# Performance work log

Measured on AMD Instinct MI355X. Metric: run time of the kernel, lower is better.

Reference implementation:

```python
import jax, jax.numpy as jnp
import numpy as np

HIDDEN = 1024
INTER = 2048
NUM_EXPERTS = 8
TOP_K = 2
GROUP_SIZE = 128
TOKENS = 4096


def _dequant_int4(packed, scale, group_size):
    # packed: [E, N, K//2] ints in [0,256) holding two uint4 nibbles (low | high<<4)
    # scale:  [E, N, K//group_size] float32
    E, N, Kh = packed.shape
    K = 2 * Kh
    low = packed & 0xF
    high = (packed >> 4) & 0xF
    # interleave: even K positions = low nibble, odd = high nibble
    q = jnp.stack([low, high], axis=-1).reshape(E, N, K) - 8  # int4 values in [-8,7]
    q = q.astype(jnp.float32).reshape(E, N, K // group_size, group_size)
    w = q * scale[..., None]
    return w.reshape(E, N, K)


def setup_inputs() -> dict:
    key = jax.random.key(0)
    k1, k2, k3, k4, k5, k6 = jax.random.split(key, 6)
    x = jax.random.normal(k1, (TOKENS, HIDDEN), dtype=jnp.float32)
    router_w = jax.random.normal(k2, (NUM_EXPERTS, HIDDEN), dtype=jnp.float32) * 0.02
    w1 = jax.random.randint(k3, (NUM_EXPERTS, 2 * INTER, HIDDEN // 2), 0, 256, dtype=jnp.int32)
    w1_scale = jax.random.uniform(k4, (NUM_EXPERTS, 2 * INTER, HIDDEN // GROUP_SIZE), dtype=jnp.float32) * 0.05
    w2 = jax.random.randint(k5, (NUM_EXPERTS, HIDDEN, INTER // 2), 0, 256, dtype=jnp.int32)
    w2_scale = jax.random.uniform(k6, (NUM_EXPERTS, HIDDEN, INTER // GROUP_SIZE), dtype=jnp.float32) * 0.05
    return {"x": x, "router_w": router_w, "w1": w1, "w1_scale": w1_scale, "w2": w2, "w2_scale": w2_scale}


def reference(x, router_w, w1, w1_scale, w2, w2_scale):
    # Router: topk then softmax over the top-k logits
    scores = x @ router_w.T                                 # [T, E]
    top_w, top_i = jax.lax.top_k(scores, TOP_K)             # [T, K]
    top_w = jax.nn.softmax(top_w, axis=-1).astype(jnp.float32)

    # Dequantize int4 grouped weights once
    w1_deq = _dequant_int4(w1, w1_scale, GROUP_SIZE)        # [E, 2I, H]
    w2_deq = _dequant_int4(w2, w2_scale, GROUP_SIZE)        # [E, H, I]

    out = jnp.zeros_like(x)
    for e in range(NUM_EXPERTS):
        # per-token routing weight for expert e (0 if not routed)
        ge = jnp.sum(top_w * (top_i == e), axis=-1)         # [T]
        h = x @ w1_deq[e].T                                  # [T, 2I]
        gate, up = h[:, :INTER], h[:, INTER:]
        a = jax.nn.silu(gate) * up                           # SwiGLU
        y = a @ w2_deq[e].T                                  # [T, H]
        out = out + ge[:, None] * y
    return out
```

## Files before the change

### kernel.cpp

```cpp
#include <hip/hip_runtime.h>
#include <hip/hip_bf16.h>

#define HIDDEN 1024
#define INTER 2048
#define NE 8
#define GS 128
#define TOKENS 4096
#define MAXROWS 9216
#define MAXTILES 72

typedef __bf16 bf16x8 __attribute__((ext_vector_type(8)));
typedef float f32x4 __attribute__((ext_vector_type(4)));

#define OFF_TOPKI 0u
#define OFF_TOPKW 32768u
#define OFF_CTRL  65536u
#define OFF_TOK   66048u
#define OFF_SLOT  102912u
#define OFF_TILE  135680u
#define OFF_XB    139776u
#define OFF_A     8530432u
#define OFF_W1D   46279168u
#define OFF_W2D   113388032u
#define OFF_Y0    OFF_W1D
#define OFF_Y1    (OFF_W1D + 18874368u)

__device__ __forceinline__ unsigned short f2bf(float f) {
  union { float f; unsigned int u; } v; v.f = f;
  unsigned int r = (v.u + 0x7FFFu + ((v.u >> 16) & 1u)) >> 16;
  return (unsigned short)r;
}
__device__ __forceinline__ float bf2f(unsigned int u) {
  union { unsigned int u; float f; } v; v.u = u << 16;
  return v.f;
}
__device__ __forceinline__ unsigned int pack2(unsigned short lo, unsigned short hi) {
  return (unsigned int)lo | ((unsigned int)hi << 16);
}

typedef const __attribute__((address_space(1))) unsigned int GAS;
typedef __attribute__((address_space(3))) unsigned int LAS;
__device__ __forceinline__ void gload16(const unsigned short* g, unsigned short* l) {
  __builtin_amdgcn_global_load_lds((GAS*)g, (LAS*)l, 16, 0, 0);
}


__global__ __launch_bounds__(256) void k_prep(const float* __restrict__ x,
    const float* __restrict__ rw, int* __restrict__ topki, float* __restrict__ topkw,
    const int* __restrict__ w1, const float* __restrict__ w1s,
    unsigned short* __restrict__ w1d,
    const int* __restrict__ w2, const float* __restrict__ w2s,
    unsigned short* __restrict__ w2d, unsigned short* __restrict__ xb) {
  int bid = blockIdx.x, tid = threadIdx.x;
  if (bid == 29696) {
    uint2 z; z.x = 0u; z.y = 0u;
    *reinterpret_cast<uint2*>(xb + (size_t)TOKENS * HIDDEN + tid * 4) = z;
    return;
  }
  if (bid >= 25600) {
    size_t idx = (size_t)(bid - 25600) * 1024 + tid * 4;
    float4 v = *reinterpret_cast<const float4*>(x + idx);
    uint2 o;
    o.x = pack2(f2bf(v.x), f2bf(v.y));
    o.y = pack2(f2bf(v.z), f2bf(v.w));
    *reinterpret_cast<uint2*>(xb + idx) = o;
    return;
  }
  if (bid >= 17408) {
    int gid = (bid - 17408) * 256 + tid;
    int i4 = gid * 4;
    int r = i4 >> 10;
    int i = i4 & 1023;
    float s = w2s[r * 16 + (i >> 6)];
    int4 p = *reinterpret_cast<const int4*>(w2 + (size_t)i4);
    int pv[4] = { p.x, p.y, p.z, p.w };
    uint4 o; unsigned int ov[4];
#pragma unroll
    for (int j = 0; j < 4; j++) {
      float lo = (float)((pv[j] & 15) - 8) * s;
      float hi = (float)(((pv[j] >> 4) & 15) - 8) * s;
      ov[j] = pack2(f2bf(lo), f2bf(hi));
    }
    o.x = ov[0]; o.y = ov[1]; o.z = ov[2]; o.w = ov[3];
    *reinterpret_cast<uint4*>(w2d + ((size_t)r << 11) + 2 * i) = o;
    return;
  }
  if (bid >= 1024) {
    int gid = (bid - 1024) * 256 + tid;
    int i4 = gid * 4;
    int r = i4 >> 9;
    int i = i4 & 511;
    float s = w1s[r * 8 + (i >> 6)];
    int4 p = *reinterpret_cast<const int4*>(w1 + (size_t)i4);
    int pv[4] = { p.x, p.y, p.z, p.w };
    uint4 o; unsigned int ov[4];
#pragma unroll
    for (int j = 0; j < 4; j++) {
      float lo = (float)((pv[j] & 15) - 8) * s;
      float hi = (float)(((pv[j] >> 4) & 15) - 8) * s;
      ov[j] = pack2(f2bf(lo), f2bf(hi));
    }
    o.x = ov[0]; o.y = ov[1]; o.z = ov[2]; o.w = ov[3];
    *reinterpret_cast<uint4*>(w1d + ((size_t)r << 10) + 2 * i) = o;
    return;
  }
  int wave = tid >> 6, lane = tid & 63;
  int t = bid * 4 + wave;
  float acc[NE];
#pragma unroll
  for (int e = 0; e < NE; e++) acc[e] = 0.f;
  const float* xr = x + (size_t)t * HIDDEN;
  for (int i = lane; i < HIDDEN; i += 64) {
    float xv = xr[i];
#pragma unroll
    for (int e = 0; e < NE; e++) acc[e] += xv * rw[e * HIDDEN + i];
  }
#pragma unroll
  for (int e = 0; e < NE; e++) {
    float v = acc[e];
    for (int off = 32; off > 0; off >>= 1) v += __shfl_down(v, off, 64);
    acc[e] = v;
  }
  if (lane == 0) {
    int b0 = 0; float s0 = acc[0];
#pragma unroll
    for (int e = 1; e < NE; e++) if (acc[e] > s0) { s0 = acc[e]; b0 = e; }
    int b1 = -1; float s1 = -3.0e38f;
#pragma unroll
    for (int e = 0; e < NE; e++) if (e != b0 && acc[e] > s1) { s1 = acc[e]; b1 = e; }
    float w0 = 1.f / (1.f + __expf(s1 - s0));
    topki[t * 2] = b0; topki[t * 2 + 1] = b1;
    topkw[t * 2] = w0; topkw[t * 2 + 1] = 1.f - w0;
  }
}

__global__ __launch_bounds__(256) void k_route2(const int* __restrict__ topki,
    int* __restrict__ ctrl, int* __restrict__ tok, int* __restrict__ slots,
    int* __restrict__ tilemap) {
  __shared__ int h[NE], off[NE], cnt[NE];
  int tid = threadIdx.x;
  if (tid < NE) h[tid] = 0;
  __syncthreads();
  for (int i = tid; i < TOKENS * 2; i += 256) atomicAdd(&h[topki[i]], 1);
  __syncthreads();
  if (tid == 0) {
    int run = 0, t = 0;
    for (int e = 0; e < NE; e++) {
      int c = h[e];
      ctrl[e] = c; ctrl[16 + e] = run; off[e] = run;
      int pc = (c + 127) & ~127;
      for (int mt = 0; mt < (pc >> 7); mt++) tilemap[t++] = (e << 20) | (run + mt * 128);
      run += pc;
    }
    ctrl[24] = run; ctrl[25] = t;
  }
  __syncthreads();
#pragma unroll
  for (int e = 0; e < NE; e++) {
    int c = h[e], pc = (c + 127) & ~127;
    for (int i = c + tid; i < pc; i += 256) tok[off[e] + i] = -1;
  }
  if (tid < NE) cnt[tid] = off[tid];
  __syncthreads();
  for (int i = tid; i < TOKENS * 2; i += 256) {
    int e = topki[i];
    int p = atomicAdd(&cnt[e], 1);
    tok[p] = i >> 1;
    slots[i] = p;
  }
}

__global__ __launch_bounds__(256) void k_gemm1(
    const unsigned short* __restrict__ xb, const unsigned short* __restrict__ w1d,
    const int* __restrict__ ctrl, const int* __restrict__ tilemap,
    const int* __restrict__ tok, unsigned short* __restrict__ a_out) {
  __shared__ unsigned short sA[128 * 32];
  __shared__ unsigned short sBg[64 * 32];
  __shared__ unsigned short sBu[64 * 32];
  int bid = blockIdx.x, tid = threadIdx.x;
  int nt = bid & 31, tile = bid >> 5;
  if (tile >= ctrl[25]) return;
  int tm = tilemap[tile];
  int e = tm >> 20, row0 = tm & 0xFFFFF;
  int n0 = nt * 64;
  int wave = tid >> 6, lane = tid & 63;
  int ln = lane & 15, quad = lane >> 4;
  int wr = (wave & 1) * 64, wc = (wave >> 1) * 32;

  int srow = tid >> 2, scblk = tid & 3;
  int scol = (scblk ^ ((srow >> 1) & 3)) * 8;
  int t0 = tok[row0 + srow];
  int t1 = tok[row0 + 64 + srow];
  const unsigned short* gA0 = xb + (size_t)(t0 < 0 ? TOKENS : t0) * HIDDEN + scol;
  const unsigned short* gA1 = xb + (size_t)(t1 < 0 ? TOKENS : t1) * HIDDEN + scol;
  const unsigned short* gBg = w1d + ((size_t)e * 4096 + n0 + srow) * HIDDEN + scol;
  const unsigned short* gBu = gBg + (size_t)INTER * HIDDEN;
  unsigned short* lA0 = sA + tid * 8;
  unsigned short* lA1 = sA + 64 * 32 + tid * 8;
  unsigned short* lBg = sBg + tid * 8;
  unsigned short* lBu = sBu + tid * 8;

  f32x4 aG[4][2] = {}, aU[4][2] = {};
  for (int k0 = 0; k0 < HIDDEN; k0 += 32) {
    __syncthreads();
    gload16(gA0 + k0, lA0);
    gload16(gA1 + k0, lA1);
    gload16(gBg + k0, lBg);
    gload16(gBu + k0, lBu);
    __syncthreads();
    bf16x8 af[4], bg[2], bu[2];
#pragma unroll
    for (int m = 0; m < 4; m++) {
      int ar = wr + m * 16 + ln;
      af[m] = *reinterpret_cast<const bf16x8*>(&sA[ar * 32 + (quad ^ ((ar >> 1) & 3)) * 8]);
    }
#pragma unroll
    for (int n = 0; n < 2; n++) {
      int br = wc + n * 16 + ln;
      int bo = br * 32 + (quad ^ ((br >> 1) & 3)) * 8;
      bg[n] = *reinterpret_cast<const bf16x8*>(&sBg[bo]);
      bu[n] = *reinterpret_cast<const bf16x8*>(&sBu[bo]);
    }
#pragma unroll
    for (int m = 0; m < 4; m++)
#pragma unroll
      for (int n = 0; n < 2; n++) {
        aG[m][n] = __builtin_amdgcn_mfma_f32_16x16x32_bf16(af[m], bg[n], aG[m][n], 0, 0, 0);
        aU[m][n] = __builtin_amdgcn_mfma_f32_16x16x32_bf16(af[m], bu[n], aU[m][n], 0, 0, 0);
      }
  }
#pragma unroll
  for (int m = 0; m < 4; m++)
#pragma unroll
    for (int n = 0; n < 2; n++) {
      int col = n0 + wc + n * 16 + ln;
#pragma unroll
      for (int r = 0; r < 4; r++) {
        float g = aG[m][n][r], u = aU[m][n][r];
        float act = (g / (1.f + __expf(-g))) * u;
        int row = row0 + wr + m * 16 + quad * 4 + r;
        a_out[(size_t)row * INTER + col] = f2bf(act);
      }
    }
}

__global__ __launch_bounds__(256) void k_gemm2(
    const unsigned short* __restrict__ a_in, const unsigned short* __restrict__ w2d,
    const int* __restrict__ ctrl, const int* __restrict__ tilemap,
    unsigned short* __restrict__ y) {
  __shared__ unsigned short sA[128 * 32];
  __shared__ unsigned short sB[128 * 32];
  int bid = blockIdx.x, tid = threadIdx.x;
  int kp = bid & 1, nt = (bid >> 1) & 7, tile = bid >> 4;
  if (tile >= ctrl[25]) return;
  int tm = tilemap[tile];
  int e = tm >> 20, row0 = tm & 0xFFFFF;
  int n0 = nt * 128;
  int wave = tid >> 6, lane = tid & 63;
  int ln = lane & 15, quad = lane >> 4;
  int wr = (wave & 1) * 64, wc = (wave >> 1) * 64;

  int srow = tid >> 2, scblk = tid & 3;
  int scol = (scblk ^ ((srow >> 1) & 3)) * 8;
  int kbase = kp * (INTER / 2);
  const unsigned short* gA0 = a_in + (size_t)(row0 + srow) * INTER + kbase + scol;
  const unsigned short* gA1 = gA0 + (size_t)64 * INTER;
  const unsigned short* gB0 = w2d + ((size_t)e * 1024 + n0 + srow) * INTER + kbase + scol;
  const unsigned short* gB1 = gB0 + (size_t)64 * INTER;
  unsigned short* lA0 = sA + tid * 8;
  unsigned short* lA1 = sA + 64 * 32 + tid * 8;
  unsigned short* lB0 = sB + tid * 8;
  unsigned short* lB1 = sB + 64 * 32 + tid * 8;

  f32x4 acc[4][4] = {};
  for (int k0 = 0; k0 < INTER / 2; k0 += 32) {
    __syncthreads();
    gload16(gA0 + k0, lA0);
    gload16(gA1 + k0, lA1);
    gload16(gB0 + k0, lB0);
    gload16(gB1 + k0, lB1);
    __syncthreads();
    bf16x8 af[4], bf_[4];
#pragma unroll
    for (int m = 0; m < 4; m++) {
      int ar = wr + m * 16 + ln;
      af[m] = *reinterpret_cast<const bf16x8*>(&sA[ar * 32 + (quad ^ ((ar >> 1) & 3)) * 8]);
    }
#pragma unroll
    for (int n = 0; n < 4; n++) {
      int br = wc + n * 16 + ln;
      bf_[n] = *reinterpret_cast<const bf16x8*>(&sB[br * 32 + (quad ^ ((br >> 1) & 3)) * 8]);
    }
#pragma unroll
    for (int m = 0; m < 4; m++)
#pragma unroll
      for (int n = 0; n < 4; n++)
        acc[m][n] = __builtin_amdgcn_mfma_f32_16x16x32_bf16(af[m], bf_[n], acc[m][n], 0, 0, 0);
  }
  unsigned short* yk = y + (size_t)kp * MAXROWS * HIDDEN;
#pragma unroll
  for (int m = 0; m < 4; m++)
#pragma unroll
    for (int n = 0; n < 4; n++) {
      int col = n0 + wc + n * 16 + ln;
#pragma unroll
      for (int r = 0; r < 4; r++) {
        int row = row0 + wr + m * 16 + quad * 4 + r;
        yk[(size_t)row * HIDDEN + col] = f2bf(acc[m][n][r]);
      }
    }
}

__global__ __launch_bounds__(256) void k_combine(const unsigned short* __restrict__ y,
    const int* __restrict__ slots, const float* __restrict__ topkw,
    float* __restrict__ out) {
  int t = blockIdx.x;
  int c = threadIdx.x * 4;
  int s0 = slots[t * 2], s1 = slots[t * 2 + 1];
  float g0 = topkw[t * 2], g1 = topkw[t * 2 + 1];
  const unsigned short* y1 = y + (size_t)MAXROWS * HIDDEN;
  uint2 a0 = *reinterpret_cast<const uint2*>(y  + (size_t)s0 * HIDDEN + c);
  uint2 a1 = *reinterpret_cast<const uint2*>(y1 + (size_t)s0 * HIDDEN + c);
  uint2 b0 = *reinterpret_cast<const uint2*>(y  + (size_t)s1 * HIDDEN + c);
  uint2 b1 = *reinterpret_cast<const uint2*>(y1 + (size_t)s1 * HIDDEN + c);
  float4 o;
  o.x = g0 * (bf2f(a0.x & 0xffffu) + bf2f(a1.x & 0xffffu))
      + g1 * (bf2f(b0.x & 0xffffu) + bf2f(b1.x & 0xffffu));
  o.y = g0 * (bf2f(a0.x >> 16) + bf2f(a1.x >> 16))
      + g1 * (bf2f(b0.x >> 16) + bf2f(b1.x >> 16));
  o.z = g0 * (bf2f(a0.y & 0xffffu) + bf2f(a1.y & 0xffffu))
      + g1 * (bf2f(b0.y & 0xffffu) + bf2f(b1.y & 0xffffu));
  o.w = g0 * (bf2f(a0.y >> 16) + bf2f(a1.y >> 16))
      + g1 * (bf2f(b0.y >> 16) + bf2f(b1.y >> 16));
  *reinterpret_cast<float4*>(out + (size_t)t * HIDDEN + c) = o;
}

extern "C" void kernel_launch(void* const* d_in, const int* in_sizes, int n_in,
                              void* d_out, int out_size, void* d_ws, size_t ws_size,
                              hipStream_t stream) {
  const float* x   = (const float*)d_in[0];
  const float* rw  = (const float*)d_in[1];
  const int*   w1  = (const int*)d_in[2];
  const float* w1s = (const float*)d_in[3];
  const int*   w2  = (const int*)d_in[4];
  const float* w2s = (const float*)d_in[5];
  float* out = (float*)d_out;
  char* ws = (char*)d_ws;

  int*   topki = (int*)(ws + OFF_TOPKI);
  float* topkw = (float*)(ws + OFF_TOPKW);
  int*   ctrl  = (int*)(ws + OFF_CTRL);
  int*   tok   = (int*)(ws + OFF_TOK);
  int*   slots = (int*)(ws + OFF_SLOT);
  int*   tilemap = (int*)(ws + OFF_TILE);
  unsigned short* xb  = (unsigned short*)(ws + OFF_XB);
  unsigned short* a   = (unsigned short*)(ws + OFF_A);
  unsigned short* w1d = (unsigned short*)(ws + OFF_W1D);
  unsigned short* w2d = (unsigned short*)(ws + OFF_W2D);
  unsigned short* y   = (unsigned short*)(ws + OFF_Y0);

  k_prep<<<29697, 256, 0, stream>>>(x, rw, topki, topkw, w1, w1s, w1d, w2, w2s, w2d, xb);
  k_route2<<<1, 256, 0, stream>>>(topki, ctrl, tok, slots, tilemap);
  k_gemm1<<<32 * MAXTILES, 256, 0, stream>>>(xb, w1d, ctrl, tilemap, tok, a);
  k_gemm2<<<16 * MAXTILES, 256, 0, stream>>>(a, w2d, ctrl, tilemap, y);
  k_combine<<<TOKENS, 256, 0, stream>>>(y, slots, topkw, out);
}
```

Before: 324.5 us.

## Rewrite gemm1 as 256x256 pipelined tile with interleaved gate/up weights

Replaces the 128x64 gemm1 tile with a 512-thread 256x256 tile. It double-buffers LDS, issues prefetches two k-steps ahead and uses setprio around the MFMA phases. The w1 dequant now interleaves gate and up rows in blocks of 16, so one B tile covers both halves, and 256-row tiles per expert are handled with a valid-row count. Routing histogram counting moves into k_prep via global atomics, and token scatter moves to a new multi-block kernel. Together these aim for more reuse per tile, latency hiding and less serial routing work, at the cost of padding waste on partial tiles and more complex synchronization.

```diff
diff --git a/kernel.cpp b/kernel.cpp
--- a/kernel.cpp
+++ b/kernel.cpp
@@ -8,6 +8,7 @@
 #define TOKENS 4096
 #define MAXROWS 9216
 #define MAXTILES 72
+#define MAXT256 40
 
 typedef __bf16 bf16x8 __attribute__((ext_vector_type(8)));
 typedef float f32x4 __attribute__((ext_vector_type(4)));
@@ -18,6 +19,8 @@
 #define OFF_TOK   66048u
 #define OFF_SLOT  102912u
 #define OFF_TILE  135680u
+#define OFF_T256  136192u
+#define OFF_V256  136448u
 #define OFF_XB    139776u
 #define OFF_A     8530432u
 #define OFF_W1D   46279168u
@@ -44,13 +47,13 @@
   __builtin_amdgcn_global_load_lds((GAS*)g, (LAS*)l, 16, 0, 0);
 }
 
-
 __global__ __launch_bounds__(256) void k_prep(const float* __restrict__ x,
     const float* __restrict__ rw, int* __restrict__ topki, float* __restrict__ topkw,
     const int* __restrict__ w1, const float* __restrict__ w1s,
     unsigned short* __restrict__ w1d,
     const int* __restrict__ w2, const float* __restrict__ w2s,
-    unsigned short* __restrict__ w2d, unsigned short* __restrict__ xb) {
+    unsigned short* __restrict__ w2d, unsigned short* __restrict__ xb,
+    int* __restrict__ ctrl) {
   int bid = blockIdx.x, tid = threadIdx.x;
   if (bid == 29696) {
     uint2 z; z.x = 0u; z.y = 0u;
@@ -101,7 +104,11 @@
       ov[j] = pack2(f2bf(lo), f2bf(hi));
     }
     o.x = ov[0]; o.y = ov[1]; o.z = ov[2]; o.w = ov[3];
-    *reinterpret_cast<uint4*>(w1d + ((size_t)r << 10) + 2 * i) = o;
+    int e = r >> 12, rr = r & 4095;
+    int tp = rr >> 11, jj = rr & 2047;
+    int il = ((jj >> 4) << 5) + (tp << 4) + (jj & 15);
+    size_t orow = ((size_t)e << 12) + il;
+    *reinterpret_cast<uint4*>(w1d + (orow << 10) + 2 * i) = o;
     return;
   }
   int wave = tid >> 6, lane = tid & 63;
@@ -131,28 +138,38 @@
     float w0 = 1.f / (1.f + __expf(s1 - s0));
     topki[t * 2] = b0; topki[t * 2 + 1] = b1;
     topkw[t * 2] = w0; topkw[t * 2 + 1] = 1.f - w0;
-  }
-}
-
-__global__ __launch_bounds__(256) void k_route2(const int* __restrict__ topki,
-    int* __restrict__ ctrl, int* __restrict__ tok, int* __restrict__ slots,
-    int* __restrict__ tilemap) {
-  __shared__ int h[NE], off[NE], cnt[NE];
+    atomicAdd(&ctrl[b0], 1);
+    atomicAdd(&ctrl[b1], 1);
+  }
+}
+
+__global__ __launch_bounds__(256) void k_route2(int* __restrict__ ctrl,
+    int* __restrict__ tok, int* __restrict__ tilemap,
+    int* __restrict__ tile256, int* __restrict__ valid256) {
+  __shared__ int h[NE], off[NE];
   int tid = threadIdx.x;
-  if (tid < NE) h[tid] = 0;
-  __syncthreads();
-  for (int i = tid; i < TOKENS * 2; i += 256) atomicAdd(&h[topki[i]], 1);
+  if (tid < NE) h[tid] = ctrl[tid];
   __syncthreads();
   if (tid == 0) {
-    int run = 0, t = 0;
+    int run = 0, t = 0, t2 = 0;
     for (int e = 0; e < NE; e++) {
       int c = h[e];
-      ctrl[e] = c; ctrl[16 + e] = run; off[e] = run;
+      ctrl[16 + e] = run; off[e] = run;
+      ctrl[8 + e] = run;
       int pc = (c + 127) & ~127;
-      for (int mt = 0; mt < (pc >> 7); mt++) tilemap[t++] = (e << 20) | (run + mt * 128);
+      int m = pc >> 7;
+      for (int mt = 0; mt < m; mt++) tilemap[t++] = (e << 20) | (run + mt * 128);
+      int n2 = (m + 1) >> 1;
+      for (int i = 0; i < n2; i++) {
+        int st = i * 256;
+        if (st + 256 > pc) st = (pc >= 256) ? (pc - 256) : 0;
+        tile256[t2] = (e << 20) | (run + st);
+        int v = pc - st; valid256[t2] = (v < 256) ? v : 256;
+        t2++;
+      }
       run += pc;
     }
-    ctrl[24] = run; ctrl[25] = t;
+    ctrl[24] = run; ctrl[25] = t; ctrl[26] = t2;
   }
   __syncthreads();
 #pragma unroll
@@ -160,88 +177,168 @@
     int c = h[e], pc = (c + 127) & ~127;
     for (int i = c + tid; i < pc; i += 256) tok[off[e] + i] = -1;
   }
-  if (tid < NE) cnt[tid] = off[tid];
+}
+
+__global__ __launch_bounds__(256) void k_scatter(const int* __restrict__ topki,
+    int* __restrict__ ctrl, int* __restrict__ tok, int* __restrict__ slots) {
+  __shared__ int lh[NE], lbase[NE];
+  int tid = threadIdx.x;
+  int i = blockIdx.x * 256 + tid;
+  if (tid < NE) lh[tid] = 0;
   __syncthreads();
-  for (int i = tid; i < TOKENS * 2; i += 256) {
-    int e = topki[i];
-    int p = atomicAdd(&cnt[e], 1);
-    tok[p] = i >> 1;
-    slots[i] = p;
-  }
-}
-
-__global__ __launch_bounds__(256) void k_gemm1(
+  int e = topki[i];
+  int lp = atomicAdd(&lh[e], 1);
+  __syncthreads();
+  if (tid < NE) lbase[tid] = lh[tid] ? atomicAdd(&ctrl[8 + tid], lh[tid]) : 0;
+  __syncthreads();
+  int p = lbase[e] + lp;
+  tok[p] = i >> 1;
+  slots[i] = p;
+}
+
+#define STAGE_A(buf, h, kt) do { \
+    const unsigned short* _g = ((h) ? pA1 : pA0) + (kt) * 64; \
+    unsigned short* _l = (unsigned short*)sA + (buf) * 16384 + (h) * 8192 + tid * 8; \
+    gload16(_g, _l); gload16(_g + 32, _l + 4096); } while (0)
+#define STAGE_B(buf, h, kt) do { \
+    const unsigned short* _g = ((h) ? pB1 : pB0) + (kt) * 64; \
+    unsigned short* _l = (unsigned short*)sB + (buf) * 16384 + (h) * 8192 + tid * 8; \
+    gload16(_g, _l); gload16(_g + 32, _l + 4096); } while (0)
+
+__global__ __launch_bounds__(512, 2) void k_gemm1(
     const unsigned short* __restrict__ xb, const unsigned short* __restrict__ w1d,
-    const int* __restrict__ ctrl, const int* __restrict__ tilemap,
-    const int* __restrict__ tok, unsigned short* __restrict__ a_out) {
-  __shared__ unsigned short sA[128 * 32];
-  __shared__ unsigned short sBg[64 * 32];
-  __shared__ unsigned short sBu[64 * 32];
+    const int* __restrict__ ctrl, const int* __restrict__ tile256,
+    const int* __restrict__ valid256, const int* __restrict__ tok,
+    unsigned short* __restrict__ a_out) {
+  __shared__ unsigned short sA[32768];
+  __shared__ unsigned short sB[32768];
   int bid = blockIdx.x, tid = threadIdx.x;
-  int nt = bid & 31, tile = bid >> 5;
-  if (tile >= ctrl[25]) return;
-  int tm = tilemap[tile];
+  int nt = bid & 15, tile = bid >> 4;
+  if (tile >= ctrl[26]) return;
+  int tm = tile256[tile];
   int e = tm >> 20, row0 = tm & 0xFFFFF;
-  int n0 = nt * 64;
-  int wave = tid >> 6, lane = tid & 63;
-  int ln = lane & 15, quad = lane >> 4;
-  int wr = (wave & 1) * 64, wc = (wave >> 1) * 32;
-
-  int srow = tid >> 2, scblk = tid & 3;
-  int scol = (scblk ^ ((srow >> 1) & 3)) * 8;
-  int t0 = tok[row0 + srow];
-  int t1 = tok[row0 + 64 + srow];
-  const unsigned short* gA0 = xb + (size_t)(t0 < 0 ? TOKENS : t0) * HIDDEN + scol;
-  const unsigned short* gA1 = xb + (size_t)(t1 < 0 ? TOKENS : t1) * HIDDEN + scol;
-  const unsigned short* gBg = w1d + ((size_t)e * 4096 + n0 + srow) * HIDDEN + scol;
-  const unsigned short* gBu = gBg + (size_t)INTER * HIDDEN;
-  unsigned short* lA0 = sA + tid * 8;
-  unsigned short* lA1 = sA + 64 * 32 + tid * 8;
-  unsigned short* lBg = sBg + tid * 8;
-  unsigned short* lBu = sBu + tid * 8;
-
-  f32x4 aG[4][2] = {}, aU[4][2] = {};
-  for (int k0 = 0; k0 < HIDDEN; k0 += 32) {
-    __syncthreads();
-    gload16(gA0 + k0, lA0);
-    gload16(gA1 + k0, lA1);
-    gload16(gBg + k0, lBg);
-    gload16(gBu + k0, lBu);
-    __syncthreads();
-    bf16x8 af[4], bg[2], bu[2];
-#pragma unroll
-    for (int m = 0; m < 4; m++) {
-      int ar = wr + m * 16 + ln;
-      af[m] = *reinterpret_cast<const bf16x8*>(&sA[ar * 32 + (quad ^ ((ar >> 1) & 3)) * 8]);
-    }
-#pragma unroll
-    for (int n = 0; n < 2; n++) {
-      int br = wc + n * 16 + ln;
-      int bo = br * 32 + (quad ^ ((br >> 1) & 3)) * 8;
-      bg[n] = *reinterpret_cast<const bf16x8*>(&sBg[bo]);
-      bu[n] = *reinterpret_cast<const bf16x8*>(&sBu[bo]);
-    }
-#pragma unroll
-    for (int m = 0; m < 4; m++)
-#pragma unroll
-      for (int n = 0; n < 2; n++) {
-        aG[m][n] = __builtin_amdgcn_mfma_f32_16x16x32_bf16(af[m], bg[n], aG[m][n], 0, 0, 0);
-        aU[m][n] = __builtin_amdgcn_mfma_f32_16x16x32_bf16(af[m], bu[n], aU[m][n], 0, 0, 0);
+  int vrows = valid256[tile];
+  int total = ctrl[24];
+  int n0 = nt * 256;
+  int wave = tid >> 6, lane = tid & 63, ln = lane & 15, quad = lane >> 4;
+  int wm = wave >> 2, wn = wave & 3;
+
+  int sr = tid >> 2;
+  int gsw = ((tid & 3) ^ ((sr >> 1) & 3)) * 8;
+  int gr0 = row0 + sr, gr1 = row0 + 128 + sr;
+  int t0 = (gr0 < total) ? tok[gr0] : -1;
+  int t1 = (gr1 < total) ? tok[gr1] : -1;
+  const unsigned short* pA0 = xb + (size_t)(t0 < 0 ? TOKENS : t0) * HIDDEN + gsw;
+  const unsigned short* pA1 = xb + (size_t)(t1 < 0 ? TOKENS : t1) * HIDDEN + gsw;
+  const unsigned short* pB0 = w1d + (((size_t)e * 4096 + n0 + sr) << 10) + gsw;
+  const unsigned short* pB1 = pB0 + ((size_t)128 << 10);
+
+  STAGE_A(0, 0, 0); STAGE_B(0, 0, 0); STAGE_B(0, 1, 0); STAGE_A(0, 1, 0);
+  STAGE_B(1, 0, 1); STAGE_B(1, 1, 1); STAGE_A(1, 0, 1);
+  asm volatile("s_waitcnt vmcnt(6)" ::: "memory");
+  __builtin_amdgcn_s_barrier();
+
+  int cb = ln * 32 + (quad ^ ((ln >> 1) & 3)) * 8;
+  int bb = (wn & 1) * 2048 + cb;
+  f32x4 acc[8][4] = {};
+  bf16x8 af[4][2], b0r[2][2], b1r[2][2];
+
+  for (int kt = 0; kt < 16; kt++) {
+    int buf = kt & 1;
+    const unsigned short* A = sA + (buf * 2 + wm) * 8192;
+    const unsigned short* B = sB + (buf * 2 + (wn >> 1)) * 8192;
+    int kn1 = (kt + 1 < 16) ? kt + 1 : 15;
+    int kn2 = (kt + 2 < 16) ? kt + 2 : 15;
+#pragma unroll
+    for (int mi = 0; mi < 4; mi++)
+#pragma unroll
+      for (int kk = 0; kk < 2; kk++)
+        af[mi][kk] = *reinterpret_cast<const bf16x8*>(A + kk * 4096 + mi * 512 + cb);
+#pragma unroll
+    for (int ni = 0; ni < 2; ni++)
+#pragma unroll
+      for (int kk = 0; kk < 2; kk++)
+        b0r[ni][kk] = *reinterpret_cast<const bf16x8*>(B + kk * 4096 + ni * 512 + bb);
+    STAGE_A(buf ^ 1, 1, kn1);
+    asm volatile("s_waitcnt lgkmcnt(8)" ::: "memory");
+    __builtin_amdgcn_s_barrier();
+    asm volatile("s_waitcnt lgkmcnt(0)" ::: "memory");
+    __builtin_amdgcn_s_setprio(1);
+#pragma unroll
+    for (int mi = 0; mi < 4; mi++)
+#pragma unroll
+      for (int ni = 0; ni < 2; ni++)
+#pragma unroll
+        for (int kk = 0; kk < 2; kk++)
+          acc[mi][ni] = __builtin_amdgcn_mfma_f32_16x16x32_bf16(af[mi][kk], b0r[ni][kk], acc[mi][ni], 0, 0, 0);
+    __builtin_amdgcn_s_setprio(0);
+    __builtin_amdgcn_s_barrier();
+#pragma unroll
+    for (int ni = 0; ni < 2; ni++)
+#pragma unroll
+      for (int kk = 0; kk < 2; kk++)
+        b1r[ni][kk] = *reinterpret_cast<const bf16x8*>(B + kk * 4096 + (2 + ni) * 512 + bb);
+    __builtin_amdgcn_s_barrier();
+    asm volatile("s_waitcnt lgkmcnt(0)" ::: "memory");
+    __builtin_amdgcn_s_setprio(1);
+#pragma unroll
+    for (int mi = 0; mi < 4; mi++)
+#pragma unroll
+      for (int ni = 0; ni < 2; ni++)
+#pragma unroll
+        for (int kk = 0; kk < 2; kk++)
+          acc[mi][2 + ni] = __builtin_amdgcn_mfma_f32_16x16x32_bf16(af[mi][kk], b1r[ni][kk], acc[mi][2 + ni], 0, 0, 0);
+    __builtin_amdgcn_s_setprio(0);
+    __builtin_amdgcn_s_barrier();
+#pragma unroll
+    for (int mi = 0; mi < 4; mi++)
+#pragma unroll
+      for (int kk = 0; kk < 2; kk++)
+        af[mi][kk] = *reinterpret_cast<const bf16x8*>(A + kk * 4096 + (4 + mi) * 512 + cb);
+    STAGE_B(buf, 0, kn2);
+    __builtin_amdgcn_s_barrier();
+    asm volatile("s_waitcnt lgkmcnt(0)" ::: "memory");
+    __builtin_amdgcn_s_setprio(1);
+#pragma unroll
+    for (int mi = 0; mi < 4; mi++)
+#pragma unroll
+      for (int ni = 0; ni < 2; ni++)
+#pragma unroll
+        for (int kk = 0; kk < 2; kk++)
+          acc[4 + mi][ni] = __builtin_amdgcn_mfma_f32_16x16x32_bf16(af[mi][kk], b0r[ni][kk], acc[4 + mi][ni], 0, 0, 0);
+    __builtin_amdgcn_s_setprio(0);
+    __builtin_amdgcn_s_barrier();
+    STAGE_B(buf, 1, kn2);
+    STAGE_A(buf, 0, kn2);
+    __builtin_amdgcn_s_barrier();
+    __builtin_amdgcn_s_setprio(1);
+#pragma unroll
+    for (int mi = 0; mi < 4; mi++)
+#pragma unroll
+      for (int ni = 0; ni < 2; ni++)
+#pragma unroll
+        for (int kk = 0; kk < 2; kk++)
+          acc[4 + mi][2 + ni] = __builtin_amdgcn_mfma_f32_16x16x32_bf16(af[mi][kk], b1r[ni][kk], acc[4 + mi][2 + ni], 0, 0, 0);
+    __builtin_amdgcn_s_setprio(0);
+    asm volatile("s_waitcnt vmcnt(6)" ::: "memory");
+    __builtin_amdgcn_s_barrier();
+  }
+  asm volatile("s_waitcnt vmcnt(0)" ::: "memory");
+
+  int jb = nt * 128 + wn * 32;
+  int rb = row0 + wm * 128;
+#pragma unroll
+  for (int mf = 0; mf < 8; mf++)
+#pragma unroll
+    for (int p = 0; p < 2; p++)
+#pragma unroll
+      for (int r = 0; r < 4; r++) {
+        float g = acc[mf][2 * p][r], u = acc[mf][2 * p + 1][r];
+        float act = (g / (1.f + __expf(-g))) * u;
+        int lr = wm * 128 + mf * 16 + quad * 4 + r;
+        if (lr < vrows)
+          a_out[(size_t)(row0 + lr) * INTER + jb + p * 16 + ln] = f2bf(act);
       }
-  }
-#pragma unroll
-  for (int m = 0; m < 4; m++)
-#pragma unroll
-    for (int n = 0; n < 2; n++) {
-      int col = n0 + wc + n * 16 + ln;
-#pragma unroll
-      for (int r = 0; r < 4; r++) {
-        float g = aG[m][n][r], u = aU[m][n][r];
-        float act = (g / (1.f + __expf(-g))) * u;
-        int row = row0 + wr + m * 16 + quad * 4 + r;
-        a_out[(size_t)row * INTER + col] = f2bf(act);
-      }
-    }
 }
 
 __global__ __launch_bounds__(256) void k_gemm2(
@@ -353,15 +450,19 @@
   int*   tok   = (int*)(ws + OFF_TOK);
   int*   slots = (int*)(ws + OFF_SLOT);
   int*   tilemap = (int*)(ws + OFF_TILE);
+  int*   tile256 = (int*)(ws + OFF_T256);
+  int*   valid256 = (int*)(ws + OFF_V256);
   unsigned short* xb  = (unsigned short*)(ws + OFF_XB);
   unsigned short* a   = (unsigned short*)(ws + OFF_A);
   unsigned short* w1d = (unsigned short*)(ws + OFF_W1D);
   unsigned short* w2d = (unsigned short*)(ws + OFF_W2D);
   unsigned short* y   = (unsigned short*)(ws + OFF_Y0);
 
-  k_prep<<<29697, 256, 0, stream>>>(x, rw, topki, topkw, w1, w1s, w1d, w2, w2s, w2d, xb);
-  k_route2<<<1, 256, 0, stream>>>(topki, ctrl, tok, slots, tilemap);
-  k_gemm1<<<32 * MAXTILES, 256, 0, stream>>>(xb, w1d, ctrl, tilemap, tok, a);
+  hipMemsetAsync(ws + OFF_CTRL, 0, 128, stream);
+  k_prep<<<29697, 256, 0, stream>>>(x, rw, topki, topkw, w1, w1s, w1d, w2, w2s, w2d, xb, ctrl);
+  k_route2<<<1, 256, 0, stream>>>(ctrl, tok, tilemap, tile256, valid256);
+  k_scatter<<<32, 256, 0, stream>>>(topki, ctrl, tok, slots);
+  k_gemm1<<<16 * MAXT256, 512, 0, stream>>>(xb, w1d, ctrl, tile256, valid256, tok, a);
   k_gemm2<<<16 * MAXTILES, 256, 0, stream>>>(a, w2d, ctrl, tilemap, y);
   k_combine<<<TOKENS, 256, 0, stream>>>(y, slots, topkw, out);
 }
```

After: 427.2 us. 31.6% more time.
